# Kernel optimization log

Measured on AMD Instinct MI355X. Metric: run time of the kernel, lower is better.

## Reference

```python
import jax, jax.numpy as jnp
import numpy as np

B, S, IN, H = 64, 512, 512, 1024


def _gru_cell(x, h, w_ih, w_hh, b_ih, b_hh):
    # PyTorch GRUCell math: gates ordered [r, z, n] along first dim of weights.
    gi = x @ w_ih.T + b_ih            # [B, 3H]
    gh = h @ w_hh.T + b_hh            # [B, 3H]
    i_r, i_z, i_n = jnp.split(gi, 3, axis=-1)
    h_r, h_z, h_n = jnp.split(gh, 3, axis=-1)
    r = jax.nn.sigmoid(i_r + h_r)
    z = jax.nn.sigmoid(i_z + h_z)
    n = jnp.tanh(i_n + r * h_n)
    return (1.0 - z) * n + z * h


def setup_inputs() -> dict:
    key = jax.random.key(0)
    ks = jax.random.split(key, 17)
    s_in = 1.0 / np.sqrt(H)
    def w(k, shape):
        return jax.random.uniform(k, shape, jnp.float32, -s_in, s_in)
    inp = {"x": jax.random.normal(ks[0], (B, S, IN), jnp.float32)}
    # layer 0 (input_size -> H), forward and backward cells
    inp["w_ih0f"] = w(ks[1], (3 * H, IN)); inp["w_hh0f"] = w(ks[2], (3 * H, H))
    inp["b_ih0f"] = w(ks[3], (3 * H,));   inp["b_hh0f"] = w(ks[4], (3 * H,))
    inp["w_ih0b"] = w(ks[5], (3 * H, IN)); inp["w_hh0b"] = w(ks[6], (3 * H, H))
    inp["b_ih0b"] = w(ks[7], (3 * H,));   inp["b_hh0b"] = w(ks[8], (3 * H,))
    # layer 1 (H -> H)
    inp["w_ih1f"] = w(ks[9], (3 * H, H));  inp["w_hh1f"] = w(ks[10], (3 * H, H))
    inp["b_ih1f"] = w(ks[11], (3 * H,));  inp["b_hh1f"] = w(ks[12], (3 * H,))
    inp["w_ih1b"] = w(ks[13], (3 * H, H)); inp["w_hh1b"] = w(ks[14], (3 * H, H))
    inp["b_ih1b"] = w(ks[15], (3 * H,));  inp["b_hh1b"] = w(ks[16], (3 * H,))
    return inp


def reference(x,
              w_ih0f, w_hh0f, b_ih0f, b_hh0f,
              w_ih0b, w_hh0b, b_ih0b, b_hh0b,
              w_ih1f, w_hh1f, b_ih1f, b_hh1f,
              w_ih1b, w_hh1b, b_ih1b, b_hh1b):
    b, hidden = x.shape[0], w_hh0f.shape[1]
    h0 = jnp.zeros((b, hidden), x.dtype)

    def step(carry, x_t):
        h0f, h0b, h1f, h1b = carry
        # NOTE: faithful to source — flip is over the FEATURE axis of the slice
        x_rev = x_t[:, ::-1]
        h0f = _gru_cell(x_t,  h0f, w_ih0f, w_hh0f, b_ih0f, b_hh0f)
        h0b = _gru_cell(x_rev, h0b, w_ih0b, w_hh0b, b_ih0b, b_hh0b)
        h1f = _gru_cell(h0f, h1f, w_ih1f, w_hh1f, b_ih1f, b_hh1f)
        h1b = _gru_cell(h0b, h1b, w_ih1b, w_hh1b, b_ih1b, b_hh1b)
        return (h0f, h0b, h1f, h1b), jnp.concatenate([h1f, h1b], axis=1)

    xs = jnp.swapaxes(x, 0, 1)  # [S, B, IN]
    _, outs = jax.lax.scan(step, (h0, h0, h0, h0), xs)
    out = jnp.swapaxes(outs, 0, 1)  # [B, S, 2H]
    return out, out[:, -1, :]
```

## Files before the change

kernel.cpp:

```cpp
#include <hip/hip_runtime.h>
#include <hip/hip_bf16.h>

typedef __attribute__((ext_vector_type(4))) float f32x4;
typedef __attribute__((ext_vector_type(8))) short short8;
typedef unsigned short u16;

constexpr int B = 64, S = 512, KIN = 512, H = 1024;

constexpr size_t OFF_CNT   = 0;
constexpr size_t OFF_H0BF  = 4096;
constexpr size_t SZ_HBF    = (size_t)2*2*B*H*2;
constexpr size_t OFF_H1BF  = OFF_H0BF + SZ_HBF;
constexpr size_t OFF_ZEND  = OFF_H1BF + SZ_HBF;
constexpr size_t OFF_XBF   = (OFF_ZEND + 255) & ~(size_t)255;
constexpr size_t SZ_XBF    = (size_t)S*B*KIN*2;
constexpr size_t OFF_WP    = OFF_XBF + SZ_XBF;
constexpr size_t WP_ELEMS0 = (size_t)64*48*1536;
constexpr size_t WP_ELEMS1 = (size_t)64*48*2048;

__device__ __forceinline__ u16 f2bf(float v) {
    __hip_bfloat16 h = __float2bfloat16(v);
    return *reinterpret_cast<u16*>(&h);
}

__global__ void pack_w(const float* __restrict__ wi0f, const float* __restrict__ wh0f,
                       const float* __restrict__ wi0b, const float* __restrict__ wh0b,
                       const float* __restrict__ wi1f, const float* __restrict__ wh1f,
                       const float* __restrict__ wi1b, const float* __restrict__ wh1b,
                       u16* __restrict__ wp) {
    int bx = blockIdx.x;
    int cell = bx / (64*48);
    int rem  = bx % (64*48);
    int blk = rem / 48, c = rem % 48;
    int K  = (cell < 2) ? 1536 : 2048;
    int Ki = (cell < 2) ? 512  : 1024;
    int n = (c >> 4)*H + blk*16 + (c & 15);
    const float* wi = (cell==0)?wi0f:(cell==1)?wi0b:(cell==2)?wi1f:wi1b;
    const float* wh = (cell==0)?wh0f:(cell==1)?wh0b:(cell==2)?wh1f:wh1b;
    size_t base = (cell==0)?0:(cell==1)?WP_ELEMS0:(cell==2)?2*WP_ELEMS0:2*WP_ELEMS0+WP_ELEMS1;
    u16* dst = wp + base + ((size_t)blk*48 + c)*K;
    for (int k = threadIdx.x; k < K; k += 256) {
        float v;
        if (k < Ki) v = wi[(size_t)n*Ki + ((cell==1) ? (Ki-1-k) : k)];
        else        v = wh[(size_t)n*H + (k - Ki)];
        dst[k] = f2bf(v);
    }
}

__global__ void conv_x(const float* __restrict__ x, u16* __restrict__ xbf) {
    int t = blockIdx.x >> 6;
    int b = blockIdx.x & 63;
    const float* src = x + ((size_t)b*S + t)*KIN;
    u16* dst = xbf + ((size_t)t*B + b)*KIN;
    for (int k = threadIdx.x; k < KIN; k += 256)
        dst[k] = f2bf(src[k]);
}

struct PArgs {
    const u16* wp;
    const u16* xbf;
    const float* bih0f; const float* bhh0f;
    const float* bih0b; const float* bhh0b;
    const float* bih1f; const float* bhh1f;
    const float* bih1b; const float* bhh1b;
    u16* h0bf; u16* h1bf;
    float* out;
    float* out2;
    unsigned* cnt;
};

#define MFMA16 __builtin_amdgcn_mfma_f32_16x16x32_bf16

template<int NKS, int NIW, int K, int LDIN>
__device__ __forceinline__ void run_cell(const PArgs& a, const int cell,
        const u16* __restrict__ wblk, const float* __restrict__ bih,
        const float* __restrict__ bhh, float (*red)[4][16][64]) {
    const int tid  = threadIdx.x;
    const int lane = tid & 63;
    const int wv   = tid >> 6;
    const int q    = lane >> 4;
    const int cix  = lane & 15;
    const int qo   = q * 8;
    const int blk  = blockIdx.x & 63;
    const int j0   = blk * 16;
    const int dir  = cell & 1;

    const int col = tid & 15;
    const int rq  = tid >> 4;
    const int r0  = rq * 4;
    const int jl  = j0 + col;
    const float br  = bih[jl]       + bhh[jl];
    const float bz  = bih[H + jl]   + bhh[H + jl];
    const float bin = bih[2*H + jl];
    const float bhn = bhh[2*H + jl];

    u16* myh0b = a.h0bf + (size_t)dir*2*B*H;
    u16* myh1b = a.h1bf + (size_t)dir*2*B*H;

    const int grp = blockIdx.x & 7;
    unsigned* gcnt = a.cnt + (size_t)grp*32;
    unsigned* root = a.cnt + (size_t)8*32;
    unsigned* flg  = a.cnt + (size_t)(9 + grp)*32;

    short8 wr[NKS], wz[NKS], wn[NKS];
    #pragma unroll
    for (int i = 0; i < NKS; ++i) {
        const int kwg = wv*NKS + i;
        wr[i] = *(const short8*)(wblk + (size_t)cix*K      + kwg*32 + qo);
        wz[i] = *(const short8*)(wblk + (size_t)(16+cix)*K + kwg*32 + qo);
        wn[i] = *(const short8*)(wblk + (size_t)(32+cix)*K + kwg*32 + qo);
    }

    float hp[4] = {0.f, 0.f, 0.f, 0.f};

    for (int tick = 0; tick <= S; ++tick) {
        const bool active = (cell < 2) ? (tick < S) : (tick >= 1);
        const int t = (cell < 2) ? tick : (tick - 1);
        if (active) {
            const int sprev = (t + 1) & 1, scur = t & 1;
            const u16* aIn;
            const u16* aHid;
            if (cell < 2) { aIn = a.xbf + (size_t)t*B*KIN;   aHid = myh0b + (size_t)sprev*B*H; }
            else          { aIn = myh0b + (size_t)scur*B*H;  aHid = myh1b + (size_t)sprev*B*H; }
            const u16* rowIn[4]; const u16* rowHid[4];
            #pragma unroll
            for (int m = 0; m < 4; ++m) {
                rowIn[m]  = aIn  + (size_t)(m*16 + cix)*LDIN + qo;
                rowHid[m] = aHid + (size_t)(m*16 + cix)*H    + qo;
            }
            f32x4 aR[4], aZ[4], aNI[4], aNH[4];
            #pragma unroll
            for (int m = 0; m < 4; ++m) {
                aR[m]  = f32x4{0,0,0,0}; aZ[m]  = f32x4{0,0,0,0};
                aNI[m] = f32x4{0,0,0,0}; aNH[m] = f32x4{0,0,0,0};
            }
            #pragma unroll
            for (int i = 0; i < NKS; ++i) {
                const int kwg = wv*NKS + i;
                if (kwg < NIW) {
                    #pragma unroll
                    for (int m = 0; m < 4; ++m) {
                        short8 af = *(const short8*)(rowIn[m] + (size_t)kwg*32);
                        aR[m]  = MFMA16(af, wr[i], aR[m],  0,0,0);
                        aZ[m]  = MFMA16(af, wz[i], aZ[m],  0,0,0);
                        aNI[m] = MFMA16(af, wn[i], aNI[m], 0,0,0);
                    }
                } else {
                    #pragma unroll
                    for (int m = 0; m < 4; ++m) {
                        short8 af = *(const short8*)(rowHid[m] + (size_t)(kwg - NIW)*32);
                        aR[m]  = MFMA16(af, wr[i], aR[m],  0,0,0);
                        aZ[m]  = MFMA16(af, wz[i], aZ[m],  0,0,0);
                        aNH[m] = MFMA16(af, wn[i], aNH[m], 0,0,0);
                    }
                }
            }
            {
                f32x4* pw = (f32x4*)&red[wv][0][0][0];
                #pragma unroll
                for (int m = 0; m < 4; ++m) {
                    const int cbase = cix*16;
                    const int csw   = (m*4 + q) ^ (cix & 7);
                    pw[0*256 + cbase + csw] = aR[m];
                    pw[1*256 + cbase + csw] = aZ[m];
                    pw[2*256 + cbase + csw] = aNI[m];
                    pw[3*256 + cbase + csw] = aNH[m];
                }
            }
            __syncthreads();
            f32x4 sR = {0,0,0,0}, sZ = {0,0,0,0}, sNI = {0,0,0,0}, sNH = {0,0,0,0};
            {
                const int cidx = col*16 + (rq ^ (col & 7));
                #pragma unroll
                for (int ww = 0; ww < 4; ++ww) {
                    const f32x4* pr = (const f32x4*)&red[ww][0][0][0];
                    sR  += pr[0*256 + cidx];
                    sZ  += pr[1*256 + cidx];
                    sNI += pr[2*256 + cidx];
                    sNH += pr[3*256 + cidx];
                }
            }
            u16* hcurb = ((cell < 2) ? myh0b : myh1b) + (size_t)scur*B*H;
            #pragma unroll
            for (int v = 0; v < 4; ++v) {
                float r  = 1.f/(1.f + __expf(-(sR[v] + br)));
                float z  = 1.f/(1.f + __expf(-(sZ[v] + bz)));
                float xn = (sNI[v] + bin) + r*(sNH[v] + bhn);
                float e2 = __expf(2.f*xn);
                float n  = 1.f - 2.f/(e2 + 1.f);
                float hn = (1.f - z)*n + z*hp[v];
                hp[v] = hn;
                __hip_atomic_store(&hcurb[(size_t)(r0 + v)*H + jl], f2bf(hn),
                                   __ATOMIC_RELAXED, __HIP_MEMORY_SCOPE_AGENT);
                if (cell >= 2) {
                    __builtin_nontemporal_store(hn, &a.out[((size_t)(r0+v)*S + t)*(2*H) + dir*H + jl]);
                    if (t == S-1)
                        __builtin_nontemporal_store(hn, &a.out2[(size_t)(r0+v)*(2*H) + dir*H + jl]);
                }
            }
        }
        if (tick < S) {
            __syncthreads();
            if (tid == 0) {
                asm volatile("s_waitcnt vmcnt(0)" ::: "memory");
                unsigned r = __hip_atomic_fetch_add(gcnt, 1u, __ATOMIC_RELAXED,
                                                    __HIP_MEMORY_SCOPE_AGENT);
                if ((r & 31u) == 31u) {
                    unsigned rr = __hip_atomic_fetch_add(root, 1u, __ATOMIC_RELAXED,
                                                         __HIP_MEMORY_SCOPE_AGENT);
                    if ((rr & 7u) == 7u) {
                        #pragma unroll
                        for (int f = 0; f < 8; ++f)
                            __hip_atomic_store(a.cnt + (size_t)(9 + f)*32, (unsigned)(tick + 1),
                                               __ATOMIC_RELAXED, __HIP_MEMORY_SCOPE_AGENT);
                    }
                }
                while (__hip_atomic_load(flg, __ATOMIC_RELAXED, __HIP_MEMORY_SCOPE_AGENT)
                       <= (unsigned)tick) {
                    __builtin_amdgcn_s_sleep(4);
                }
                __builtin_amdgcn_fence(__ATOMIC_ACQUIRE, "agent");
            }
            __syncthreads();
        }
    }
}

__launch_bounds__(256, 1)
__global__ void gru_persist(PArgs a) {
    __shared__ __align__(16) float red[4][4][16][64];
    const int cell = blockIdx.x >> 6;
    const int blk  = blockIdx.x & 63;
    if (cell == 0) {
        run_cell<12,16,1536,KIN>(a, 0, a.wp + (size_t)blk*48*1536,
                                 a.bih0f, a.bhh0f, red);
    } else if (cell == 1) {
        run_cell<12,16,1536,KIN>(a, 1, a.wp + WP_ELEMS0 + (size_t)blk*48*1536,
                                 a.bih0b, a.bhh0b, red);
    } else if (cell == 2) {
        run_cell<16,32,2048,H>(a, 2, a.wp + 2*WP_ELEMS0 + (size_t)blk*48*2048,
                               a.bih1f, a.bhh1f, red);
    } else {
        run_cell<16,32,2048,H>(a, 3, a.wp + 2*WP_ELEMS0 + WP_ELEMS1 + (size_t)blk*48*2048,
                               a.bih1b, a.bhh1b, red);
    }
}

extern "C" void kernel_launch(void* const* d_in, const int* in_sizes, int n_in,
                              void* d_out, int out_size, void* d_ws, size_t ws_size,
                              hipStream_t stream) {
    const float* x    = (const float*)d_in[0];
    const float* wi0f = (const float*)d_in[1];
    const float* wh0f = (const float*)d_in[2];
    const float* bi0f = (const float*)d_in[3];
    const float* bh0f = (const float*)d_in[4];
    const float* wi0b = (const float*)d_in[5];
    const float* wh0b = (const float*)d_in[6];
    const float* bi0b = (const float*)d_in[7];
    const float* bh0b = (const float*)d_in[8];
    const float* wi1f = (const float*)d_in[9];
    const float* wh1f = (const float*)d_in[10];
    const float* bi1f = (const float*)d_in[11];
    const float* bh1f = (const float*)d_in[12];
    const float* wi1b = (const float*)d_in[13];
    const float* wh1b = (const float*)d_in[14];
    const float* bi1b = (const float*)d_in[15];
    const float* bh1b = (const float*)d_in[16];

    char* ws = (char*)d_ws;
    hipMemsetAsync(ws, 0, OFF_ZEND, stream);

    u16* xbf = (u16*)(ws + OFF_XBF);
    u16* wp  = (u16*)(ws + OFF_WP);

    pack_w<<<4*64*48, 256, 0, stream>>>(wi0f, wh0f, wi0b, wh0b, wi1f, wh1f, wi1b, wh1b, wp);
    conv_x<<<S*B, 256, 0, stream>>>(x, xbf);

    PArgs a;
    a.wp = wp; a.xbf = xbf;
    a.bih0f = bi0f; a.bhh0f = bh0f; a.bih0b = bi0b; a.bhh0b = bh0b;
    a.bih1f = bi1f; a.bhh1f = bh1f; a.bih1b = bi1b; a.bhh1b = bh1b;
    a.h0bf = (u16*)(ws + OFF_H0BF); a.h1bf = (u16*)(ws + OFF_H1BF);
    a.out  = (float*)d_out;
    a.out2 = (float*)d_out + (size_t)B*S*2*H;
    a.cnt  = (unsigned*)(ws + OFF_CNT);
    gru_persist<<<256, 256, 0, stream>>>(a);
}
```

Measured before the change: 8.228 ms.

## Double waves per block, split h-store and output-store paths, flatten grid barrier

Raises the persistent kernel to 512 threads (8 waves) so each wave handles half as many K-slices, and does a two-stage LDS reduction where waves 4-7 hand partials to waves 0-3. The upper 256 threads compute the gate math again and write the fp32 output, while the lower 256 write the bf16 hidden state, so the two stores run in parallel. The hierarchical counter/flag barrier becomes a flat scheme: each block increments its group counter and spins until all 8 counters reach the target, which removes one level of latency but adds more polling traffic. Hidden-state reads now use relaxed atomic 64-bit loads instead of relying on an acquire fence, which may change how the loads are cached.

```diff
diff --git a/kernel.cpp b/kernel.cpp
--- a/kernel.cpp
+++ b/kernel.cpp
@@ -4,6 +4,7 @@
 typedef __attribute__((ext_vector_type(4))) float f32x4;
 typedef __attribute__((ext_vector_type(8))) short short8;
 typedef unsigned short u16;
+typedef unsigned long long u64;
 
 constexpr int B = 64, S = 512, KIN = 512, H = 1024;
 
@@ -21,6 +22,14 @@
 __device__ __forceinline__ u16 f2bf(float v) {
     __hip_bfloat16 h = __float2bfloat16(v);
     return *reinterpret_cast<u16*>(&h);
+}
+
+__device__ __forceinline__ short8 ldh16(const u16* p) {
+    u64 lo = __hip_atomic_load((const u64*)p,       __ATOMIC_RELAXED, __HIP_MEMORY_SCOPE_AGENT);
+    u64 hi = __hip_atomic_load((const u64*)p + 1,   __ATOMIC_RELAXED, __HIP_MEMORY_SCOPE_AGENT);
+    union { u64 q[2]; short8 s; } u;
+    u.q[0] = lo; u.q[1] = hi;
+    return u.s;
 }
 
 __global__ void pack_w(const float* __restrict__ wi0f, const float* __restrict__ wh0f,
@@ -71,10 +80,10 @@
 
 #define MFMA16 __builtin_amdgcn_mfma_f32_16x16x32_bf16
 
-template<int NKS, int NIW, int K, int LDIN>
+template<int NKS, int NIW, int K, int LDIN, bool INATM>
 __device__ __forceinline__ void run_cell(const PArgs& a, const int cell,
         const u16* __restrict__ wblk, const float* __restrict__ bih,
-        const float* __restrict__ bhh, float (*red)[4][16][64]) {
+        const float* __restrict__ bhh, f32x4* red) {
     const int tid  = threadIdx.x;
     const int lane = tid & 63;
     const int wv   = tid >> 6;
@@ -86,9 +95,10 @@
     const int dir  = cell & 1;
 
     const int col = tid & 15;
-    const int rq  = tid >> 4;
+    const int rq  = (tid >> 4) & 15;
     const int r0  = rq * 4;
     const int jl  = j0 + col;
+    const bool hPath = (tid < 256);
     const float br  = bih[jl]       + bhh[jl];
     const float bz  = bih[H + jl]   + bhh[H + jl];
     const float bin = bih[2*H + jl];
@@ -99,8 +109,6 @@
 
     const int grp = blockIdx.x & 7;
     unsigned* gcnt = a.cnt + (size_t)grp*32;
-    unsigned* root = a.cnt + (size_t)8*32;
-    unsigned* flg  = a.cnt + (size_t)(9 + grp)*32;
 
     short8 wr[NKS], wz[NKS], wn[NKS];
     #pragma unroll
@@ -140,7 +148,9 @@
                 if (kwg < NIW) {
                     #pragma unroll
                     for (int m = 0; m < 4; ++m) {
-                        short8 af = *(const short8*)(rowIn[m] + (size_t)kwg*32);
+                        short8 af;
+                        if (INATM) af = ldh16(rowIn[m] + (size_t)kwg*32);
+                        else       af = *(const short8*)(rowIn[m] + (size_t)kwg*32);
                         aR[m]  = MFMA16(af, wr[i], aR[m],  0,0,0);
                         aZ[m]  = MFMA16(af, wz[i], aZ[m],  0,0,0);
                         aNI[m] = MFMA16(af, wn[i], aNI[m], 0,0,0);
@@ -148,15 +158,15 @@
                 } else {
                     #pragma unroll
                     for (int m = 0; m < 4; ++m) {
-                        short8 af = *(const short8*)(rowHid[m] + (size_t)(kwg - NIW)*32);
+                        short8 af = ldh16(rowHid[m] + (size_t)(kwg - NIW)*32);
                         aR[m]  = MFMA16(af, wr[i], aR[m],  0,0,0);
                         aZ[m]  = MFMA16(af, wz[i], aZ[m],  0,0,0);
                         aNH[m] = MFMA16(af, wn[i], aNH[m], 0,0,0);
                     }
                 }
             }
-            {
-                f32x4* pw = (f32x4*)&red[wv][0][0][0];
+            if (wv >= 4) {
+                f32x4* pw = red + (size_t)(wv - 4)*1024;
                 #pragma unroll
                 for (int m = 0; m < 4; ++m) {
                     const int cbase = cix*16;
@@ -168,34 +178,52 @@
                 }
             }
             __syncthreads();
-            f32x4 sR = {0,0,0,0}, sZ = {0,0,0,0}, sNI = {0,0,0,0}, sNH = {0,0,0,0};
-            {
+            if (wv < 4) {
+                f32x4* pw = red + (size_t)wv*1024;
+                #pragma unroll
+                for (int m = 0; m < 4; ++m) {
+                    const int cbase = cix*16;
+                    const int csw   = (m*4 + q) ^ (cix & 7);
+                    aR[m]  += pw[0*256 + cbase + csw];
+                    aZ[m]  += pw[1*256 + cbase + csw];
+                    aNI[m] += pw[2*256 + cbase + csw];
+                    aNH[m] += pw[3*256 + cbase + csw];
+                    pw[0*256 + cbase + csw] = aR[m];
+                    pw[1*256 + cbase + csw] = aZ[m];
+                    pw[2*256 + cbase + csw] = aNI[m];
+                    pw[3*256 + cbase + csw] = aNH[m];
+                }
+            }
+            __syncthreads();
+            if (hPath || cell >= 2) {
+                f32x4 sR = {0,0,0,0}, sZ = {0,0,0,0}, sNI = {0,0,0,0}, sNH = {0,0,0,0};
                 const int cidx = col*16 + (rq ^ (col & 7));
                 #pragma unroll
                 for (int ww = 0; ww < 4; ++ww) {
-                    const f32x4* pr = (const f32x4*)&red[ww][0][0][0];
+                    const f32x4* pr = red + (size_t)ww*1024;
                     sR  += pr[0*256 + cidx];
                     sZ  += pr[1*256 + cidx];
                     sNI += pr[2*256 + cidx];
                     sNH += pr[3*256 + cidx];
                 }
-            }
-            u16* hcurb = ((cell < 2) ? myh0b : myh1b) + (size_t)scur*B*H;
-            #pragma unroll
-            for (int v = 0; v < 4; ++v) {
-                float r  = 1.f/(1.f + __expf(-(sR[v] + br)));
-                float z  = 1.f/(1.f + __expf(-(sZ[v] + bz)));
-                float xn = (sNI[v] + bin) + r*(sNH[v] + bhn);
-                float e2 = __expf(2.f*xn);
-                float n  = 1.f - 2.f/(e2 + 1.f);
-                float hn = (1.f - z)*n + z*hp[v];
-                hp[v] = hn;
-                __hip_atomic_store(&hcurb[(size_t)(r0 + v)*H + jl], f2bf(hn),
-                                   __ATOMIC_RELAXED, __HIP_MEMORY_SCOPE_AGENT);
-                if (cell >= 2) {
-                    __builtin_nontemporal_store(hn, &a.out[((size_t)(r0+v)*S + t)*(2*H) + dir*H + jl]);
-                    if (t == S-1)
-                        __builtin_nontemporal_store(hn, &a.out2[(size_t)(r0+v)*(2*H) + dir*H + jl]);
+                u16* hcurb = ((cell < 2) ? myh0b : myh1b) + (size_t)scur*B*H;
+                #pragma unroll
+                for (int v = 0; v < 4; ++v) {
+                    float r  = 1.f/(1.f + __expf(-(sR[v] + br)));
+                    float z  = 1.f/(1.f + __expf(-(sZ[v] + bz)));
+                    float xn = (sNI[v] + bin) + r*(sNH[v] + bhn);
+                    float e2 = __expf(2.f*xn);
+                    float n  = 1.f - 2.f/(e2 + 1.f);
+                    float hn = (1.f - z)*n + z*hp[v];
+                    hp[v] = hn;
+                    if (hPath) {
+                        __hip_atomic_store(&hcurb[(size_t)(r0 + v)*H + jl], f2bf(hn),
+                                           __ATOMIC_RELAXED, __HIP_MEMORY_SCOPE_AGENT);
+                    } else {
+                        __builtin_nontemporal_store(hn, &a.out[((size_t)(r0+v)*S + t)*(2*H) + dir*H + jl]);
+                        if (t == S-1)
+                            __builtin_nontemporal_store(hn, &a.out2[(size_t)(r0+v)*(2*H) + dir*H + jl]);
+                    }
                 }
             }
         }
@@ -203,46 +231,40 @@
             __syncthreads();
             if (tid == 0) {
                 asm volatile("s_waitcnt vmcnt(0)" ::: "memory");
-                unsigned r = __hip_atomic_fetch_add(gcnt, 1u, __ATOMIC_RELAXED,
-                                                    __HIP_MEMORY_SCOPE_AGENT);
-                if ((r & 31u) == 31u) {
-                    unsigned rr = __hip_atomic_fetch_add(root, 1u, __ATOMIC_RELAXED,
-                                                         __HIP_MEMORY_SCOPE_AGENT);
-                    if ((rr & 7u) == 7u) {
-                        #pragma unroll
-                        for (int f = 0; f < 8; ++f)
-                            __hip_atomic_store(a.cnt + (size_t)(9 + f)*32, (unsigned)(tick + 1),
-                                               __ATOMIC_RELAXED, __HIP_MEMORY_SCOPE_AGENT);
-                    }
-                }
-                while (__hip_atomic_load(flg, __ATOMIC_RELAXED, __HIP_MEMORY_SCOPE_AGENT)
-                       <= (unsigned)tick) {
-                    __builtin_amdgcn_s_sleep(4);
-                }
-                __builtin_amdgcn_fence(__ATOMIC_ACQUIRE, "agent");
+                __hip_atomic_fetch_add(gcnt, 1u, __ATOMIC_RELAXED, __HIP_MEMORY_SCOPE_AGENT);
+                const unsigned tgt = 32u*(unsigned)(tick + 1);
+                for (;;) {
+                    bool ok = true;
+                    #pragma unroll
+                    for (int f = 0; f < 8; ++f)
+                        ok &= (__hip_atomic_load(a.cnt + (size_t)f*32, __ATOMIC_RELAXED,
+                                                 __HIP_MEMORY_SCOPE_AGENT) >= tgt);
+                    if (ok) break;
+                    __builtin_amdgcn_s_sleep(2);
+                }
             }
             __syncthreads();
         }
     }
 }
 
-__launch_bounds__(256, 1)
+__launch_bounds__(512, 2)
 __global__ void gru_persist(PArgs a) {
-    __shared__ __align__(16) float red[4][4][16][64];
+    __shared__ __align__(16) f32x4 red[4096];
     const int cell = blockIdx.x >> 6;
     const int blk  = blockIdx.x & 63;
     if (cell == 0) {
-        run_cell<12,16,1536,KIN>(a, 0, a.wp + (size_t)blk*48*1536,
-                                 a.bih0f, a.bhh0f, red);
+        run_cell<6,16,1536,KIN,false>(a, 0, a.wp + (size_t)blk*48*1536,
+                                      a.bih0f, a.bhh0f, red);
     } else if (cell == 1) {
-        run_cell<12,16,1536,KIN>(a, 1, a.wp + WP_ELEMS0 + (size_t)blk*48*1536,
-                                 a.bih0b, a.bhh0b, red);
+        run_cell<6,16,1536,KIN,false>(a, 1, a.wp + WP_ELEMS0 + (size_t)blk*48*1536,
+                                      a.bih0b, a.bhh0b, red);
     } else if (cell == 2) {
-        run_cell<16,32,2048,H>(a, 2, a.wp + 2*WP_ELEMS0 + (size_t)blk*48*2048,
-                               a.bih1f, a.bhh1f, red);
+        run_cell<8,32,2048,H,true>(a, 2, a.wp + 2*WP_ELEMS0 + (size_t)blk*48*2048,
+                                   a.bih1f, a.bhh1f, red);
     } else {
-        run_cell<16,32,2048,H>(a, 3, a.wp + 2*WP_ELEMS0 + WP_ELEMS1 + (size_t)blk*48*2048,
-                               a.bih1b, a.bhh1b, red);
+        run_cell<8,32,2048,H,true>(a, 3, a.wp + 2*WP_ELEMS0 + WP_ELEMS1 + (size_t)blk*48*2048,
+                                   a.bih1b, a.bhh1b, red);
     }
 }
 
@@ -284,5 +306,5 @@
     a.out  = (float*)d_out;
     a.out2 = (float*)d_out + (size_t)B*S*2*H;
     a.cnt  = (unsigned*)(ws + OFF_CNT);
-    gru_persist<<<256, 256, 0, stream>>>(a);
-}
+    gru_persist<<<256, 512, 0, stream>>>(a);
+}
```

Measured after the change: 11.15 ms. 1.36x slower.
